# Performance work log

Hardware: AMD Instinct MI355X
Metric: run time of the kernel (lower is better)

Reference implementation:

```python
import jax, jax.numpy as jnp
import numpy as np

B, TP, TH = 128, 128, 64
V, E, H, O = 50000, 300, 512, 3


def _lstm(x, lens, Wih, Whh, bih, bhh):
    # PyTorch LSTM, batch_first, gate order i,f,g,o; masked like pack_padded_sequence
    Bn, T, _ = x.shape
    Hn = Whh.shape[1]
    mask = jnp.arange(T)[None, :] < lens[:, None]  # [B,T]
    def step(carry, xt_mt):
        h, c = carry
        xt, mt = xt_mt  # [B,E], [B,1]
        g = xt @ Wih.T + h @ Whh.T + bih + bhh
        i, f, gg, o = jnp.split(g, 4, axis=-1)
        c_new = jax.nn.sigmoid(f) * c + jax.nn.sigmoid(i) * jnp.tanh(gg)
        h_new = jax.nn.sigmoid(o) * jnp.tanh(c_new)
        return (jnp.where(mt, h_new, h), jnp.where(mt, c_new, c)), jnp.where(mt, h_new, 0.0)
    z = jnp.zeros((Bn, Hn), x.dtype)
    _, hs = jax.lax.scan(step, (z, z), (jnp.swapaxes(x, 0, 1), jnp.swapaxes(mask, 0, 1)[..., None]))
    return jnp.swapaxes(hs, 0, 1)  # [B,T,H]


def _cell(x, h, c, Wih, Whh, bih, bhh):
    g = x @ Wih.T + h @ Whh.T + bih + bhh
    i, f, gg, o = jnp.split(g, 4, axis=-1)
    c_new = jax.nn.sigmoid(f) * c + jax.nn.sigmoid(i) * jnp.tanh(gg)
    h_new = jax.nn.sigmoid(o) * jnp.tanh(c_new)
    return h_new, c_new


def setup_inputs() -> dict:
    key = jax.random.key(0)
    ks = jax.random.split(key, 24)
    def unif(k, shape, fan):
        s = 1.0 / np.sqrt(fan)
        return jax.random.uniform(k, shape, jnp.float32, -s, s)
    inp = {}
    inp["premise"] = jax.random.randint(ks[0], (B, TP), 0, V, jnp.int32)
    inp["premise_len"] = jnp.full((B,), TP, jnp.int32)
    inp["hypothesis"] = jax.random.randint(ks[1], (B, TH), 0, V, jnp.int32)
    inp["hypothesis_len"] = jnp.full((B,), TH, jnp.int32)
    inp["embed_table"] = jax.random.normal(ks[2], (V, E), jnp.float32) * 0.1
    inp["embed_table"] = inp["embed_table"].at[0].set(0.0)  # padding_idx=0
    # premise LSTM
    inp["Wih_p"] = unif(ks[3], (4 * H, E), H); inp["Whh_p"] = unif(ks[4], (4 * H, H), H)
    inp["bih_p"] = unif(ks[5], (4 * H,), H); inp["bhh_p"] = unif(ks[6], (4 * H,), H)
    # hypothesis LSTM
    inp["Wih_h"] = unif(ks[7], (4 * H, E), H); inp["Whh_h"] = unif(ks[8], (4 * H, H), H)
    inp["bih_h"] = unif(ks[9], (4 * H,), H); inp["bhh_h"] = unif(ks[10], (4 * H,), H)
    # match LSTMCell (input 2H)
    inp["Wih_m"] = unif(ks[11], (4 * H, 2 * H), H); inp["Whh_m"] = unif(ks[12], (4 * H, H), H)
    inp["bih_m"] = unif(ks[13], (4 * H,), H); inp["bhh_m"] = unif(ks[14], (4 * H,), H)
    # attention
    inp["w_e"] = jax.random.uniform(ks[15], (H,), jnp.float32, 0.0, 1.0)
    inp["W_s"] = unif(ks[16], (H, H), H)
    inp["W_t"] = unif(ks[17], (H, H), H)
    inp["W_m"] = unif(ks[18], (H, H), H)
    inp["W_fc"] = unif(ks[19], (O, H), H)
    inp["b_fc"] = unif(ks[20], (O,), H)
    return inp


def reference(premise, premise_len, hypothesis, hypothesis_len, embed_table,
              Wih_p, Whh_p, bih_p, bhh_p, Wih_h, Whh_h, bih_h, bhh_h,
              Wih_m, Whh_m, bih_m, bhh_m, w_e, W_s, W_t, W_m, W_fc, b_fc):
    Bn = premise.shape[0]
    Hn = Whh_m.shape[1]
    p_emb = embed_table[premise]      # [B,Tp,E]
    h_emb = embed_table[hypothesis]   # [B,Th,E]
    h_s = _lstm(p_emb, premise_len, Wih_p, Whh_p, bih_p, bhh_p)      # [B,Tp,H]
    h_t = _lstm(h_emb, hypothesis_len, Wih_h, Whh_h, bih_h, bhh_h)   # [B,Th,H]
    Ws = jnp.einsum('bth,gh->btg', h_s, W_s)  # precompute w_s(h_s) once

    def step(carry, htk):
        h_m, c_m = carry
        q = htk @ W_t.T + h_m @ W_m.T                    # [B,H]
        s = jnp.tanh(Ws + q[:, None, :])                 # [B,Tp,H]
        e = s @ w_e                                      # [B,Tp]
        alpha = jax.nn.softmax(e, axis=1)                # softmax over premise positions
        a = jnp.einsum('bt,bth->bh', alpha, h_s)
        m_k = jnp.concatenate([a, htk], axis=1)          # [B,2H]
        h_m2, c_m2 = _cell(m_k, h_m, c_m, Wih_m, Whh_m, bih_m, bhh_m)
        return (h_m2, c_m2), h_m2

    z = jnp.zeros((Bn, Hn), h_s.dtype)
    _, hm_all = jax.lax.scan(step, (z, z), jnp.swapaxes(h_t, 0, 1))  # [Th,B,H]
    hm_all = jnp.swapaxes(hm_all, 0, 1)                              # [B,Th,H]
    idx = (hypothesis_len - 1).astype(jnp.int32)[:, None, None]
    last = jnp.take_along_axis(hm_all, idx, axis=1)[:, 0, :]         # last hidden per example
    return last @ W_fc.T + b_fc
```

## Files before the change

### kernel.cpp

```cpp
#include <hip/hip_runtime.h>

constexpr int BB = 128;
constexpr int TPp = 128;
constexpr int THh = 64;
constexpr int HH = 512;

constexpr size_t OFF_HS     = 0;
constexpr size_t SZ_HS      = (size_t)16384 * 512;
constexpr size_t OFF_HT     = OFF_HS + SZ_HS;
constexpr size_t SZ_HT      = (size_t)8192 * 512;
constexpr size_t OFF_WSM    = OFF_HT + SZ_HT;
constexpr size_t SZ_WSM     = (size_t)16384 * 512;
constexpr size_t OFF_WIHT_P = OFF_WSM + SZ_WSM;
constexpr size_t SZ_WIHT    = (size_t)304 * 2048;
constexpr size_t OFF_WIHT_H = OFF_WIHT_P + SZ_WIHT;
constexpr size_t OFF_WHHT_P = OFF_WIHT_H + SZ_WIHT;
constexpr size_t OFF_WHHT_H = OFF_WHHT_P + (size_t)512 * 2048;
constexpr size_t OFF_WB1T   = OFF_WHHT_H + (size_t)512 * 2048;
constexpr size_t OFF_WIA    = OFF_WB1T + (size_t)2560 * 1024;
constexpr size_t OFF_WEF    = OFF_WIA + (size_t)2048 * 512;
constexpr size_t OFF_BM     = OFF_WEF + 512;
constexpr size_t OFF_HC_P   = OFF_BM + 2048;
constexpr size_t OFF_HC_H   = OFF_HC_P + 2 * (size_t)BB * HH;
constexpr size_t OFF_C_P    = OFF_HC_H + 2 * (size_t)BB * HH;
constexpr size_t OFF_C_H    = OFF_C_P + (size_t)BB * HH;
constexpr size_t OFF_Q      = OFF_C_H + (size_t)BB * HH;
constexpr size_t OFF_GH     = OFF_Q + (size_t)BB * HH;
constexpr size_t OFF_A      = OFF_GH + (size_t)BB * 2048;
constexpr size_t OFF_HM     = OFF_A + (size_t)BB * HH;
constexpr size_t OFF_CM     = OFF_HM + (size_t)BB * HH;
constexpr size_t OFF_LAST   = OFF_CM + (size_t)BB * HH;
constexpr size_t OFF_BARP   = OFF_LAST + (size_t)BB * HH;
constexpr size_t OFF_BARH   = OFF_BARP + 2560;
constexpr size_t OFF_BARF   = OFF_BARH + 2560;
constexpr size_t OFF_BARM   = OFF_BARF + 4352;
constexpr size_t WS_FLOATS  = OFF_BARM + 4352;

__device__ __forceinline__ float sigmf(float x) { return 1.0f / (1.0f + __expf(-x)); }
__device__ __forceinline__ float tanh_f(float x) {
  float e = __expf(-2.0f * fabsf(x));
  float r = (1.0f - e) / (1.0f + e);
  return copysignf(r, x);
}

__device__ __forceinline__ float aload4(const float* p) {
  unsigned u = __hip_atomic_load((const unsigned*)p, __ATOMIC_RELAXED, __HIP_MEMORY_SCOPE_AGENT);
  return __uint_as_float(u);
}
__device__ __forceinline__ void astore4(float* p, float v) {
  __hip_atomic_store((unsigned*)p, __float_as_uint(v), __ATOMIC_RELAXED, __HIP_MEMORY_SCOPE_AGENT);
}
__device__ __forceinline__ float4 aload16(const float* p) {
  const unsigned long long* q = (const unsigned long long*)p;
  unsigned long long u0 = __hip_atomic_load(q, __ATOMIC_RELAXED, __HIP_MEMORY_SCOPE_AGENT);
  unsigned long long u1 = __hip_atomic_load(q + 1, __ATOMIC_RELAXED, __HIP_MEMORY_SCOPE_AGENT);
  union { unsigned long long u; float2 f; } c0, c1;
  c0.u = u0; c1.u = u1;
  float4 f; f.x = c0.f.x; f.y = c0.f.y; f.z = c1.f.x; f.w = c1.f.y;
  return f;
}

__device__ __forceinline__ void gbar3(unsigned* bar, int ep, int base, int n) {
  asm volatile("s_waitcnt vmcnt(0) lgkmcnt(0)" ::: "memory");
  __syncthreads();
  const int tid = threadIdx.x;
  const int rel = (int)blockIdx.x - base;
  if (tid == 0)
    __hip_atomic_store(bar + (size_t)rel * 16, (unsigned)ep,
                       __ATOMIC_RELAXED, __HIP_MEMORY_SCOPE_AGENT);
  if (rel == 0) {
    for (int s = tid; s < n; s += (int)blockDim.x)
      while (__hip_atomic_load(bar + (size_t)s * 16,
                               __ATOMIC_RELAXED, __HIP_MEMORY_SCOPE_AGENT) < (unsigned)ep)
        __builtin_amdgcn_s_sleep(1);
    __syncthreads();
    if (tid == 0)
      __hip_atomic_store(bar + (size_t)n * 16, (unsigned)ep,
                         __ATOMIC_RELAXED, __HIP_MEMORY_SCOPE_AGENT);
  } else if (tid == 0) {
    while (__hip_atomic_load(bar + (size_t)n * 16,
                             __ATOMIC_RELAXED, __HIP_MEMORY_SCOPE_AGENT) < (unsigned)ep)
      __builtin_amdgcn_s_sleep(1);
  }
  __syncthreads();
}

__global__ void k_diag(float* out, float v) {
  int i = blockIdx.x * 64 + threadIdx.x;
  if (i < BB * 3) out[i] = v;
}

__global__ __launch_bounds__(256) void k_prep(float* ws,
    const float* Wih_p, const float* bih_p, const float* bhh_p,
    const float* Wih_h, const float* bih_h, const float* bhh_h,
    const float* Whh_p, const float* Whh_h,
    const float* Whh_m, const float* Wih_m, const float* bih_m, const float* bhh_m,
    const float* W_m, const float* W_t, const float* w_e) {
  size_t gid = (size_t)blockIdx.x * 256 + threadIdx.x;
  if (gid < SZ_WIHT) {
    int k = (int)(gid >> 11), r = (int)(gid & 2047);
    float v = (k < 300) ? Wih_p[(size_t)r * 300 + k]
            : (k == 303) ? (bih_p[r] + bhh_p[r]) : 0.f;
    ws[OFF_WIHT_P + gid] = v;
    return;
  }
  gid -= SZ_WIHT;
  if (gid < SZ_WIHT) {
    int k = (int)(gid >> 11), r = (int)(gid & 2047);
    float v = (k < 300) ? Wih_h[(size_t)r * 300 + k]
            : (k == 303) ? (bih_h[r] + bhh_h[r]) : 0.f;
    ws[OFF_WIHT_H + gid] = v;
    return;
  }
  gid -= SZ_WIHT;
  const size_t NT = (size_t)512 * 2048;
  if (gid < NT) {
    int li = (int)(gid >> 13);
    int rem = (int)(gid & 8191);
    int k = rem >> 4, c = rem & 15;
    int jj = c >> 2, g = c & 3;
    ws[OFF_WHHT_P + gid] = Whh_p[(size_t)(g * 512 + li * 4 + jj) * 512 + k];
    return;
  }
  gid -= NT;
  if (gid < NT) {
    int li = (int)(gid >> 13);
    int rem = (int)(gid & 8191);
    int k = rem >> 4, c = rem & 15;
    int jj = c >> 2, g = c & 3;
    ws[OFF_WHHT_H + gid] = Whh_h[(size_t)(g * 512 + li * 4 + jj) * 512 + k];
    return;
  }
  gid -= NT;
  if (gid < (size_t)2560 * 1024) {
    int c = (int)(gid >> 10), k = (int)(gid & 1023);
    float v;
    if (c < 512) {
      v = (k < 512) ? W_m[(size_t)c * 512 + k] : W_t[(size_t)c * 512 + (k - 512)];
    } else {
      int p = c - 512;
      int j = p >> 2, g = p & 3;
      int r = g * 512 + j;
      v = (k < 512) ? Whh_m[(size_t)r * 512 + k] : Wih_m[(size_t)r * 1024 + k];
    }
    ws[OFF_WB1T + gid] = v;
    return;
  }
  gid -= (size_t)2560 * 1024;
  if (gid < (size_t)2048 * 512) {
    int c = (int)(gid >> 9), k = (int)(gid & 511);
    int j = c >> 2, g = c & 3;
    ws[OFF_WIA + gid] = Wih_m[((size_t)g * 512 + j) * 1024 + k];
    return;
  }
  gid -= (size_t)2048 * 512;
  if (gid < 512) { ws[OFF_WEF + gid] = w_e[gid]; return; }
  gid -= 512;
  if (gid < 2048) { ws[OFF_BM + gid] = bih_m[gid] + bhh_m[gid]; return; }
  gid -= 2048;
  if (gid < (size_t)393216) { ws[OFF_HC_P + gid] = 0.f; return; }
  gid -= 393216;
  if (gid < (size_t)131072) { ws[OFF_HM + gid] = 0.f; return; }
  gid -= 131072;
  if (gid < 13824) { ws[OFF_BARP + gid] = 0.f; return; }
}

__global__ __launch_bounds__(256) void k_gemm(const float* __restrict__ A,
                                              const float* __restrict__ Bw, int ldb, int Kdim,
                                              int N, float* __restrict__ C, int ntilesN) {
  __shared__ float As[16][68];
  __shared__ float Bs[16][68];
  const int tid = threadIdx.x;
  const int bid = blockIdx.x;
  const int tm = bid / ntilesN, tn = bid % ntilesN;
  const int m0 = tm * 64, n0 = tn * 64;
  const int tx = tid & 15, ty = tid >> 4;
  const int srow = tid >> 2, skc = (tid & 3) * 4;
  float acc[4][4] = {};
  const float* arowf = A + (size_t)(m0 + srow) * Kdim;
  const float* brow = Bw + (size_t)(n0 + srow) * ldb;
  for (int k0 = 0; k0 < Kdim; k0 += 16) {
    float4 v = *(const float4*)(arowf + k0 + skc);
    As[skc + 0][srow] = v.x; As[skc + 1][srow] = v.y;
    As[skc + 2][srow] = v.z; As[skc + 3][srow] = v.w;
#pragma unroll
    for (int i = 0; i < 4; i++) Bs[skc + i][srow] = brow[k0 + skc + i];
    __syncthreads();
#pragma unroll
    for (int kk = 0; kk < 16; kk++) {
      float4 a4 = *(float4*)&As[kk][ty * 4];
      float4 b4 = *(float4*)&Bs[kk][tx * 4];
      acc[0][0] += a4.x * b4.x; acc[0][1] += a4.x * b4.y; acc[0][2] += a4.x * b4.z; acc[0][3] += a4.x * b4.w;
      acc[1][0] += a4.y * b4.x; acc[1][1] += a4.y * b4.y; acc[1][2] += a4.y * b4.z; acc[1][3] += a4.y * b4.w;
      acc[2][0] += a4.z * b4.x; acc[2][1] += a4.z * b4.y; acc[2][2] += a4.z * b4.z; acc[2][3] += a4.z * b4.w;
      acc[3][0] += a4.w * b4.x; acc[3][1] += a4.w * b4.y; acc[3][2] += a4.w * b4.z; acc[3][3] += a4.w * b4.w;
    }
    __syncthreads();
  }
  const int m = m0 + ty * 4, n = n0 + tx * 4;
#pragma unroll
  for (int i = 0; i < 4; i++) {
    float4 o = {acc[i][0], acc[i][1], acc[i][2], acc[i][3]};
    *(float4*)&C[(size_t)(m + i) * N + n] = o;
  }
}

__global__ __launch_bounds__(512) void k_lstm_mega(float* __restrict__ ws,
    const int* __restrict__ premise, const int* __restrict__ hyp,
    const int* __restrict__ plen, const int* __restrict__ hlen,
    const float* __restrict__ emb) {
  __shared__ float4 wlds4[2048];
  __shared__ float4 scr4[2048];
  float* Bx = (float*)wlds4;
  float* Alds = (float*)scr4;

  const int tid = threadIdx.x;
  const int bid = blockIdx.x;
  const int seq = bid >> 7;
  const int li = bid & 127;
  const int T = seq ? THh : TPp;
  const int* toks = seq ? hyp : premise;
  const int* lens = seq ? hlen : plen;
  const float* wstk = ws + (seq ? OFF_WHHT_H : OFF_WHHT_P) + (size_t)li * 8192;
  const float* WX = ws + (seq ? OFF_WIHT_H : OFF_WIHT_P);
  float* hc = ws + (seq ? OFF_HC_H : OFF_HC_P);
  float* xg = ws + OFF_WSM + (size_t)bid * 32768;
  unsigned* barS = (unsigned*)(ws + (seq ? OFF_BARH : OFF_BARP));
  const int sbase = seq ? 128 : 0;

  const int w = tid >> 6, lane = tid & 63;
  const int cg = w & 3, bh = w >> 2;
  const int b = bh * 64 + lane;
  const int sw = b & 7;
  const int jcol = li * 4 + cg;
  const int len = lens[b];
  float c_r = 0.f, h_r = 0.f;
  int epS = 1;
  int sb[4], sk[4];
#pragma unroll
  for (int j2 = 0; j2 < 4; j2++) { int fi = tid + j2 * 512; sb[j2] = fi >> 4; sk[j2] = fi & 15; }
  const int kofs = (tid & 3) * 4;

  for (int t = 0; t < T; t++) {
    if ((t & 15) == 0) {
      __syncthreads();
      for (int i = tid; i < 16 * 304; i += 512) {
        int c = i / 304, kk = i - c * 304;
        int jj = c >> 2, g = c & 3;
        Bx[i] = WX[(size_t)kk * 2048 + g * 512 + li * 4 + jj];
      }
      __syncthreads();
      for (int rg = 0; rg < 4; rg++) {
        int tk[4];
#pragma unroll
        for (int j2 = 0; j2 < 4; j2++) {
          int rl = (tid >> 2) + j2 * 128;
          int R = rg * 512 + rl;
          int tl = R >> 7, bb = R & 127;
          tk[j2] = toks[(size_t)bb * T + t + tl];
        }
        float4 pa[4];
#pragma unroll
        for (int j2 = 0; j2 < 4; j2++) {
          if (kofs + 3 < 300) pa[j2] = *(const float4*)(emb + (size_t)tk[j2] * 300 + kofs);
          else { float4 z = {0.f, 0.f, 0.f, 0.f}; pa[j2] = z; }
        }
        float acc[16];
#pragma unroll
        for (int c = 0; c < 16; c++) acc[c] = 0.f;
        for (int ck = 0; ck < 19; ck++) {
          __syncthreads();
#pragma unroll
          for (int j2 = 0; j2 < 4; j2++) {
            int fi = tid + j2 * 512;
            *(float4*)&Alds[(fi >> 2) * 16 + kofs] = pa[j2];
          }
          __syncthreads();
          if (ck < 18) {
            int kb = (ck + 1) * 16 + kofs;
#pragma unroll
            for (int j2 = 0; j2 < 4; j2++) {
              if (kb + 3 < 300) {
                pa[j2] = *(const float4*)(emb + (size_t)tk[j2] * 300 + kb);
              } else {
                float v0 = (kb + 0 < 300) ? emb[(size_t)tk[j2] * 300 + kb + 0] : (kb + 0 == 303 ? 1.f : 0.f);
                float v1 = (kb + 1 < 300) ? emb[(size_t)tk[j2] * 300 + kb + 1] : (kb + 1 == 303 ? 1.f : 0.f);
                float v2 = (kb + 2 < 300) ? emb[(size_t)tk[j2] * 300 + kb + 2] : (kb + 2 == 303 ? 1.f : 0.f);
                float v3 = (kb + 3 < 300) ? emb[(size_t)tk[j2] * 300 + kb + 3] : (kb + 3 == 303 ? 1.f : 0.f);
                float4 z = {v0, v1, v2, v3}; pa[j2] = z;
              }
            }
          }
          int kb0 = ck * 16;
#pragma unroll
          for (int kk4 = 0; kk4 < 4; kk4++) {
            float4 av = *(float4*)&Alds[tid * 16 + kk4 * 4];
#pragma unroll
            for (int c = 0; c < 16; c++) {
              float4 bv = *(float4*)&Bx[c * 304 + kb0 + kk4 * 4];
              acc[c] += av.x * bv.x + av.y * bv.y + av.z * bv.z + av.w * bv.w;
            }
          }
        }
        int R = rg * 512 + tid;
#pragma unroll
        for (int cq = 0; cq < 4; cq++) {
          float4 o = {acc[cq * 4], acc[cq * 4 + 1], acc[cq * 4 + 2], acc[cq * 4 + 3]};
          *(float4*)&xg[(size_t)R * 16 + cq * 4] = o;
        }
      }
      __syncthreads();
      {
        const float4* src = (const float4*)wstk;
#pragma unroll
        for (int j2 = 0; j2 < 4; j2++) wlds4[tid + j2 * 512] = src[tid + j2 * 512];
      }
    }
    {
      const int par = t & 1;
      const float* hin = hc + (size_t)par * (BB * HH);
      float* hout = hc + (size_t)(par ^ 1) * (BB * HH);
      float4 acc = {0.f, 0.f, 0.f, 0.f};
      float4 pre[4];
#pragma unroll
      for (int j2 = 0; j2 < 4; j2++)
        pre[j2] = aload16(hin + (size_t)sb[j2] * 512 + sk[j2] * 4);
      for (int kc = 0; kc < 512; kc += 64) {
        __syncthreads();
#pragma unroll
        for (int j2 = 0; j2 < 4; j2++)
          scr4[sb[j2] * 16 + (sk[j2] ^ (sb[j2] & 7))] = pre[j2];
        __syncthreads();
        if (kc + 64 < 512) {
#pragma unroll
          for (int j2 = 0; j2 < 4; j2++)
            pre[j2] = aload16(hin + (size_t)sb[j2] * 512 + (kc + 64) + sk[j2] * 4);
        }
#pragma unroll
        for (int kk = 0; kk < 64; kk += 4) {
          int k4 = kk >> 2;
          float4 h4 = scr4[b * 16 + (k4 ^ sw)];
          float4 w0 = wlds4[(kc + kk + 0) * 4 + cg];
          float4 w1 = wlds4[(kc + kk + 1) * 4 + cg];
          float4 w2 = wlds4[(kc + kk + 2) * 4 + cg];
          float4 w3 = wlds4[(kc + kk + 3) * 4 + cg];
          acc.x += h4.x * w0.x + h4.y * w1.x + h4.z * w2.x + h4.w * w3.x;
          acc.y += h4.x * w0.y + h4.y * w1.y + h4.z * w2.y + h4.w * w3.y;
          acc.z += h4.x * w0.z + h4.y * w1.z + h4.z * w2.z + h4.w * w3.z;
          acc.w += h4.x * w0.w + h4.y * w1.w + h4.z * w2.w + h4.w * w3.w;
        }
      }
      float4 x0 = *(const float4*)&xg[(((size_t)(t & 15)) * 128 + b) * 16 + cg * 4];
      float iv = sigmf(acc.x + x0.x), fv = sigmf(acc.y + x0.y);
      float gv = tanh_f(acc.z + x0.z), ov = sigmf(acc.w + x0.w);
      float cn = fv * c_r + iv * gv;
      float hn = ov * tanh_f(cn);
      bool inr = t < len;
      if (inr) { c_r = cn; h_r = hn; }
      if (!seq) ws[OFF_HS + ((size_t)b * TPp + t) * 512 + jcol] = inr ? hn : 0.f;
      else      ws[OFF_HT + ((size_t)b * THh + t) * 512 + jcol] = inr ? hn : 0.f;
      astore4(hout + (size_t)b * 512 + jcol, h_r);
      gbar3(barS, epS, sbase, 128); epS++;
    }
  }
}

__global__ __launch_bounds__(512) void k_match_mega(float* __restrict__ ws,
                                                    const int* __restrict__ hlen) {
  __shared__ float smem[16384];
  float* B1 = smem;
  float* W3 = smem + 10240;
  float4* AL4 = (float4*)(smem + 14336);
  float* SCR = smem + 14336;

  const int tid = threadIdx.x;
  const int bid = blockIdx.x;
  float* hm = ws + OFF_HM;
  const float* ht = ws + OFF_HT;
  float* qT = ws + OFF_Q;
  float* ghT = ws + OFF_GH;
  float* abuf = ws + OFF_A;
  float* last = ws + OFF_LAST;
  unsigned* barM = (unsigned*)(ws + OFF_BARM);

  {
    const float* src = ws + OFF_WB1T + (size_t)bid * 10240;
    for (int i = tid; i < 10240; i += 512) B1[i] = src[i];
    const float* s2 = ws + OFF_WIA + (size_t)bid * 4096;
    for (int i = tid; i < 4096; i += 512) W3[i] = s2[i];
  }
  const int r = tid & 127;
  const int khh = (tid >> 7) & 1;
  const int h5 = tid >> 8;
  const int j3 = bid * 2 + h5;
  const int skh = tid >> 8, sq4 = (tid >> 7) & 1, sbv = tid & 127;
  float c_reg = 0.f;
  float bmp[4];
#pragma unroll
  for (int g = 0; g < 4; g++) bmp[g] = ws[OFF_BM + g * 512 + j3];
  const int hl = hlen[r];
  int ep = 1;
  __syncthreads();

  for (int k = 0; k < THh; k++) {
    {
      float acc[5] = {0.f, 0.f, 0.f, 0.f, 0.f};
      float4 p = (skh == 0) ? aload16(&hm[(size_t)sbv * 512 + sq4 * 4])
                            : *(const float4*)&ht[((size_t)sbv * THh + k) * 512 + sq4 * 4];
      for (int ch = 0; ch < 64; ch++) {
        __syncthreads();
        AL4[skh * 256 + sq4 * 128 + sbv] = p;
        __syncthreads();
        if (ch < 63) {
          int kn = (ch + 1) * 8 + sq4 * 4;
          p = (skh == 0) ? aload16(&hm[(size_t)sbv * 512 + kn])
                         : *(const float4*)&ht[((size_t)sbv * THh + k) * 512 + kn];
        }
        const int kb = khh * 512 + ch * 8;
#pragma unroll
        for (int q4 = 0; q4 < 2; q4++) {
          float4 av = AL4[khh * 256 + q4 * 128 + r];
#pragma unroll
          for (int cc = 0; cc < 5; cc++) {
            float4 bv = *(float4*)&B1[(h5 * 5 + cc) * 1024 + kb + q4 * 4];
            acc[cc] += av.x * bv.x + av.y * bv.y + av.z * bv.z + av.w * bv.w;
          }
        }
      }
      __syncthreads();
      if (khh == 1) {
#pragma unroll
        for (int cc = 0; cc < 5; cc++) SCR[(h5 * 5 + cc) * 128 + r] = acc[cc];
      }
      __syncthreads();
      if (khh == 0) {
#pragma unroll
        for (int cc = 0; cc < 5; cc++) {
          float val = acc[cc] + SCR[(h5 * 5 + cc) * 128 + r];
          int c = bid * 10 + h5 * 5 + cc;
          if (c < 512) astore4(&qT[(size_t)c * 128 + r], val);
          else astore4(&ghT[(size_t)(c - 512) * 128 + r], val);
        }
      }
    }
    gbar3(barM, ep, 0, 256); ep++;
    if (bid < 128) {
      float* q_lds = SCR; float* we_lds = SCR + 512; float* e_part = SCR + 1024;
      float* e_lds = SCR + 1536; float* alpha_lds = SCR + 1664; float* red_s = SCR + 1792;
      const int b = bid;
      const float* Wsb = ws + OFF_WSM;
      const float* hs = ws + OFF_HS;
      q_lds[tid] = aload4(&qT[(size_t)tid * 128 + b]);
      we_lds[tid] = ws[OFF_WEF + tid];
      __syncthreads();
      {
        int t2 = tid >> 2;
        int gbase = (tid & 3) * 128;
        const float* wsrow = Wsb + ((size_t)b * TPp + t2) * 512 + gbase;
        float s = 0.f;
        for (int ii = 0; ii < 128; ii += 4) {
          float4 wv = *(const float4*)(wsrow + ii);
          float4 qv = *(float4*)&q_lds[gbase + ii];
          float4 ev = *(float4*)&we_lds[gbase + ii];
          s += tanh_f(wv.x + qv.x) * ev.x + tanh_f(wv.y + qv.y) * ev.y +
               tanh_f(wv.z + qv.z) * ev.z + tanh_f(wv.w + qv.w) * ev.w;
        }
        e_part[tid] = s;
      }
      __syncthreads();
      if (tid < 128)
        e_lds[tid] = e_part[tid * 4] + e_part[tid * 4 + 1] + e_part[tid * 4 + 2] + e_part[tid * 4 + 3];
      __syncthreads();
      if (tid < 64) {
        float m = fmaxf(e_lds[tid], e_lds[tid + 64]);
        for (int off = 32; off > 0; off >>= 1) m = fmaxf(m, __shfl_down(m, off));
        if (tid == 0) red_s[0] = m;
      }
      __syncthreads();
      if (tid < 128) alpha_lds[tid] = __expf(e_lds[tid] - red_s[0]);
      __syncthreads();
      if (tid < 64) {
        float s = alpha_lds[tid] + alpha_lds[tid + 64];
        for (int off = 32; off > 0; off >>= 1) s += __shfl_down(s, off);
        if (tid == 0) red_s[1] = 1.f / s;
      }
      __syncthreads();
      {
        float inv = red_s[1];
        float a0 = 0.f;
        const float* hsb = hs + (size_t)b * TPp * 512 + tid;
        for (int t2 = 0; t2 < TPp; t2++) a0 += alpha_lds[t2] * hsb[(size_t)t2 * 512];
        astore4(&abuf[(size_t)b * 512 + tid], a0 * inv);
      }
    }
    gbar3(barM, ep, 0, 256); ep++;
    {
      float acc3[4] = {0.f, 0.f, 0.f, 0.f};
      float4 p3 = aload16(&abuf[(size_t)sbv * 512 + skh * 256 + sq4 * 4]);
      for (int ch = 0; ch < 32; ch++) {
        __syncthreads();
        AL4[skh * 256 + sq4 * 128 + sbv] = p3;
        __syncthreads();
        if (ch < 31) {
          int kn = skh * 256 + (ch + 1) * 8 + sq4 * 4;
          p3 = aload16(&abuf[(size_t)sbv * 512 + kn]);
        }
        const int kb = khh * 256 + ch * 8;
#pragma unroll
        for (int q4 = 0; q4 < 2; q4++) {
          float4 av = AL4[khh * 256 + q4 * 128 + r];
#pragma unroll
          for (int cc = 0; cc < 4; cc++) {
            float4 wv = *(float4*)&W3[(h5 * 4 + cc) * 512 + kb + q4 * 4];
            acc3[cc] += av.x * wv.x + av.y * wv.y + av.z * wv.z + av.w * wv.w;
          }
        }
      }
      __syncthreads();
      if (khh == 1) {
#pragma unroll
        for (int cc = 0; cc < 4; cc++) SCR[(h5 * 4 + cc) * 128 + r] = acc3[cc];
      }
      __syncthreads();
      if (khh == 0) {
        float g4[4];
#pragma unroll
        for (int g = 0; g < 4; g++) {
          g4[g] = acc3[g] + SCR[(h5 * 4 + g) * 128 + r] +
                  aload4(&ghT[(size_t)(j3 * 4 + g) * 128 + r]) + bmp[g];
        }
        float iv = sigmf(g4[0]), fv = sigmf(g4[1]), gg = tanh_f(g4[2]), ov = sigmf(g4[3]);
        float cn = fv * c_reg + iv * gg;
        float hn = ov * tanh_f(cn);
        c_reg = cn;
        astore4(&hm[(size_t)r * 512 + j3], hn);
        if (k == hl - 1) last[(size_t)r * 512 + j3] = hn;
      }
    }
    gbar3(barM, ep, 0, 256); ep++;
  }
}

__global__ __launch_bounds__(256) void k_fc(const float* __restrict__ ws, const float* __restrict__ Wfc,
                                            const float* __restrict__ bfc, float* __restrict__ out) {
  int idx = blockIdx.x * 256 + threadIdx.x;
  if (idx >= BB * 3) return;
  int b = idx / 3, o = idx - b * 3;
  const float* lrow = ws + OFF_LAST + (size_t)b * 512;
  const float* wrow = Wfc + (size_t)o * 512;
  float acc = bfc[o];
  for (int h = 0; h < 512; h++) acc += lrow[h] * wrow[h];
  out[idx] = acc;
}

extern "C" void kernel_launch(void* const* d_in, const int* in_sizes, int n_in, void* d_out,
                              int out_size, void* d_ws, size_t ws_size, hipStream_t stream) {
  const int* premise = (const int*)d_in[0];
  const int* plen = (const int*)d_in[1];
  const int* hyp = (const int*)d_in[2];
  const int* hlen = (const int*)d_in[3];
  const float* emb = (const float*)d_in[4];
  const float* Wih_p = (const float*)d_in[5];
  const float* Whh_p = (const float*)d_in[6];
  const float* bih_p = (const float*)d_in[7];
  const float* bhh_p = (const float*)d_in[8];
  const float* Wih_h = (const float*)d_in[9];
  const float* Whh_h = (const float*)d_in[10];
  const float* bih_h = (const float*)d_in[11];
  const float* bhh_h = (const float*)d_in[12];
  const float* Wih_m = (const float*)d_in[13];
  const float* Whh_m = (const float*)d_in[14];
  const float* bih_m = (const float*)d_in[15];
  const float* bhh_m = (const float*)d_in[16];
  const float* w_e = (const float*)d_in[17];
  const float* W_s = (const float*)d_in[18];
  const float* W_t = (const float*)d_in[19];
  const float* W_m = (const float*)d_in[20];
  const float* W_fc = (const float*)d_in[21];
  const float* b_fc = (const float*)d_in[22];
  float* ws = (float*)d_ws;
  float* out = (float*)d_out;

  if (ws_size < WS_FLOATS * sizeof(float)) {
    float mb = (float)((double)ws_size / (1024.0 * 1024.0));
    k_diag<<<dim3(6), dim3(64), 0, stream>>>(out, mb);
    return;
  }

  {
    size_t total = 2 * SZ_WIHT + 2 * (size_t)512 * 2048 + (size_t)2560 * 1024 +
                   (size_t)2048 * 512 + 512 + 2048 + 393216 + 131072 + 13824;
    int nb = (int)((total + 255) / 256);
    k_prep<<<dim3(nb), dim3(256), 0, stream>>>(ws, Wih_p, bih_p, bhh_p, Wih_h, bih_h, bhh_h,
                                               Whh_p, Whh_h, Whh_m, Wih_m, bih_m, bhh_m,
                                               W_m, W_t, w_e);
  }
  {
    void* args[] = {(void*)&ws, (void*)&premise, (void*)&hyp, (void*)&plen, (void*)&hlen, (void*)&emb};
    hipError_t e = hipLaunchCooperativeKernel((const void*)k_lstm_mega, dim3(256), dim3(512),
                                              args, 0, stream);
    if (e != hipSuccess)
      k_lstm_mega<<<dim3(256), dim3(512), 0, stream>>>(ws, premise, hyp, plen, hlen, emb);
  }
  k_gemm<<<dim3(256 * 8), dim3(256), 0, stream>>>(ws + OFF_HS, W_s, 512, 512, 512,
                                                  ws + OFF_WSM, 8);
  {
    void* args[] = {(void*)&ws, (void*)&hlen};
    hipError_t e = hipLaunchCooperativeKernel((const void*)k_match_mega, dim3(256), dim3(512),
                                              args, 0, stream);
    if (e != hipSuccess)
      k_match_mega<<<dim3(256), dim3(512), 0, stream>>>(ws, hlen);
  }
  k_fc<<<dim3(2), dim3(256), 0, stream>>>(ws, W_fc, b_fc, out);
}
```

Baseline: 11.81 ms.

## Partition recurrent kernels by batch groups with local barriers instead of global

Both persistent kernels (LSTM and match) are re-partitioned so each block group owns a slice of batch rows (16 rows) and a slice of gate columns. Grid barriers then only span the 16 or 32 blocks of a group instead of all 128 or 256 blocks, since batch rows are independent. Recurrent weights are now streamed from global/L2 each step instead of kept resident in LDS. The input projection is computed cooperatively as a tiled GEMM across the group. The goal is lower barrier latency per timestep, paid for with more global weight traffic per step.

Measured after the change: 13.06 ms. 10.6% more time.

```diff
diff --git a/kernel.cpp b/kernel.cpp
--- a/kernel.cpp
+++ b/kernel.cpp
@@ -59,18 +59,25 @@
   float4 f; f.x = c0.f.x; f.y = c0.f.y; f.z = c1.f.x; f.w = c1.f.y;
   return f;
 }
-
-__device__ __forceinline__ void gbar3(unsigned* bar, int ep, int base, int n) {
+__device__ __forceinline__ void astore16(float* p, float4 v) {
+  union { unsigned long long u; float2 f; } c0, c1;
+  c0.f.x = v.x; c0.f.y = v.y; c1.f.x = v.z; c1.f.y = v.w;
+  unsigned long long* q = (unsigned long long*)p;
+  __hip_atomic_store(q, c0.u, __ATOMIC_RELAXED, __HIP_MEMORY_SCOPE_AGENT);
+  __hip_atomic_store(q + 1, c1.u, __ATOMIC_RELAXED, __HIP_MEMORY_SCOPE_AGENT);
+}
+
+__device__ __forceinline__ void gbarD(unsigned* bar, int ep, int first, int n) {
   asm volatile("s_waitcnt vmcnt(0) lgkmcnt(0)" ::: "memory");
   __syncthreads();
   const int tid = threadIdx.x;
-  const int rel = (int)blockIdx.x - base;
+  const int rel = (int)blockIdx.x - first;
   if (tid == 0)
     __hip_atomic_store(bar + (size_t)rel * 16, (unsigned)ep,
                        __ATOMIC_RELAXED, __HIP_MEMORY_SCOPE_AGENT);
   if (rel == 0) {
-    for (int s = tid; s < n; s += (int)blockDim.x)
-      while (__hip_atomic_load(bar + (size_t)s * 16,
+    if (tid < n)
+      while (__hip_atomic_load(bar + (size_t)tid * 16,
                                __ATOMIC_RELAXED, __HIP_MEMORY_SCOPE_AGENT) < (unsigned)ep)
         __builtin_amdgcn_s_sleep(1);
     __syncthreads();
@@ -83,6 +90,12 @@
       __builtin_amdgcn_s_sleep(1);
   }
   __syncthreads();
+}
+
+__device__ __forceinline__ float red4(float v) {
+  v += __shfl_down(v, 16, 64);
+  v += __shfl_down(v, 32, 64);
+  return v;
 }
 
 __global__ void k_diag(float* out, float v) {
@@ -115,20 +128,16 @@
   gid -= SZ_WIHT;
   const size_t NT = (size_t)512 * 2048;
   if (gid < NT) {
-    int li = (int)(gid >> 13);
-    int rem = (int)(gid & 8191);
-    int k = rem >> 4, c = rem & 15;
-    int jj = c >> 2, g = c & 3;
-    ws[OFF_WHHT_P + gid] = Whh_p[(size_t)(g * 512 + li * 4 + jj) * 512 + k];
+    int c = (int)(gid >> 9), kk = (int)(gid & 511);
+    int j = c >> 2, g = c & 3;
+    ws[OFF_WHHT_P + gid] = Whh_p[(size_t)(g * 512 + j) * 512 + kk];
     return;
   }
   gid -= NT;
   if (gid < NT) {
-    int li = (int)(gid >> 13);
-    int rem = (int)(gid & 8191);
-    int k = rem >> 4, c = rem & 15;
-    int jj = c >> 2, g = c & 3;
-    ws[OFF_WHHT_H + gid] = Whh_h[(size_t)(g * 512 + li * 4 + jj) * 512 + k];
+    int c = (int)(gid >> 9), kk = (int)(gid & 511);
+    int j = c >> 2, g = c & 3;
+    ws[OFF_WHHT_H + gid] = Whh_h[(size_t)(g * 512 + j) * 512 + kk];
     return;
   }
   gid -= NT;
@@ -209,248 +218,223 @@
     const int* __restrict__ premise, const int* __restrict__ hyp,
     const int* __restrict__ plen, const int* __restrict__ hlen,
     const float* __restrict__ emb) {
-  __shared__ float4 wlds4[2048];
-  __shared__ float4 scr4[2048];
-  float* Bx = (float*)wlds4;
-  float* Alds = (float*)scr4;
+  __shared__ float4 smem4[4096];
+  float4* Alds4 = smem4;
+  float* xAs = (float*)(smem4 + 2048);
+  float* xBs = xAs + 16 * 68;
+  int* xTok = (int*)(xBs + 16 * 68);
 
   const int tid = threadIdx.x;
   const int bid = blockIdx.x;
   const int seq = bid >> 7;
-  const int li = bid & 127;
+  const int u = bid & 127;
+  const int gb = u >> 4, gj = u & 15;
   const int T = seq ? THh : TPp;
   const int* toks = seq ? hyp : premise;
   const int* lens = seq ? hlen : plen;
-  const float* wstk = ws + (seq ? OFF_WHHT_H : OFF_WHHT_P) + (size_t)li * 8192;
+  const float* WL = ws + (seq ? OFF_WHHT_H : OFF_WHHT_P);
   const float* WX = ws + (seq ? OFF_WIHT_H : OFF_WIHT_P);
   float* hc = ws + (seq ? OFF_HC_H : OFF_HC_P);
-  float* xg = ws + OFF_WSM + (size_t)bid * 32768;
-  unsigned* barS = (unsigned*)(ws + (seq ? OFF_BARH : OFF_BARP));
-  const int sbase = seq ? 128 : 0;
+  float* hsout = ws + (seq ? OFF_HT : OFF_HS);
+  float* xgd = ws + OFF_WSM + (size_t)(seq * 8 + gb) * (16 * 16 * 2048);
+  unsigned* bar = (unsigned*)(ws + (seq ? OFF_BARH : OFF_BARP)) + gb * 272;
+  const int dfirst = seq * 128 + gb * 16;
 
   const int w = tid >> 6, lane = tid & 63;
-  const int cg = w & 3, bh = w >> 2;
-  const int b = bh * 64 + lane;
-  const int sw = b & 7;
-  const int jcol = li * 4 + cg;
-  const int len = lens[b];
-  float c_r = 0.f, h_r = 0.f;
-  int epS = 1;
-  int sb[4], sk[4];
-#pragma unroll
-  for (int j2 = 0; j2 < 4; j2++) { int fi = tid + j2 * 512; sb[j2] = fi >> 4; sk[j2] = fi & 15; }
-  const int kofs = (tid & 3) * 4;
+  const int b_loc = lane & 15, kq = lane >> 4;
+  const int b_glob = gb * 16 + b_loc;
+  const int c0 = gj * 128 + w * 16;
+  const int j0 = c0 >> 2;
+  const int len = lens[b_glob];
+  float c_r[4] = {0.f, 0.f, 0.f, 0.f}, h_r[4] = {0.f, 0.f, 0.f, 0.f};
+  int ep = 1;
 
   for (int t = 0; t < T; t++) {
     if ((t & 15) == 0) {
-      __syncthreads();
-      for (int i = tid; i < 16 * 304; i += 512) {
-        int c = i / 304, kk = i - c * 304;
-        int jj = c >> 2, g = c & 3;
-        Bx[i] = WX[(size_t)kk * 2048 + g * 512 + li * 4 + jj];
-      }
-      __syncthreads();
-      for (int rg = 0; rg < 4; rg++) {
-        int tk[4];
-#pragma unroll
-        for (int j2 = 0; j2 < 4; j2++) {
-          int rl = (tid >> 2) + j2 * 128;
-          int R = rg * 512 + rl;
-          int tl = R >> 7, bb = R & 127;
-          tk[j2] = toks[(size_t)bb * T + t + tl];
-        }
-        float4 pa[4];
-#pragma unroll
-        for (int j2 = 0; j2 < 4; j2++) {
-          if (kofs + 3 < 300) pa[j2] = *(const float4*)(emb + (size_t)tk[j2] * 300 + kofs);
-          else { float4 z = {0.f, 0.f, 0.f, 0.f}; pa[j2] = z; }
-        }
-        float acc[16];
-#pragma unroll
-        for (int c = 0; c < 16; c++) acc[c] = 0.f;
-        for (int ck = 0; ck < 19; ck++) {
-          __syncthreads();
-#pragma unroll
-          for (int j2 = 0; j2 < 4; j2++) {
-            int fi = tid + j2 * 512;
-            *(float4*)&Alds[(fi >> 2) * 16 + kofs] = pa[j2];
+      for (int ti = gj; ti < 128; ti += 16) {
+        const int tm = ti >> 5, tn = ti & 31;
+        const int m0 = tm * 64, n0 = tn * 64;
+        if (tid < 64) {
+          int rr = m0 + tid;
+          int tl = rr >> 4, bl = rr & 15;
+          xTok[tid] = toks[(size_t)(gb * 16 + bl) * T + t + tl];
+        }
+        __syncthreads();
+        const int sr = tid & 63, sk2 = (tid >> 6) * 2;
+        const int tx = tid & 15, ty = tid >> 4;
+        float acc2[2][4] = {};
+        for (int k0 = 0; k0 < 304; k0 += 16) {
+          int tok = xTok[sr];
+#pragma unroll
+          for (int i = 0; i < 2; i++) {
+            int kx = k0 + sk2 + i;
+            float v = 0.f;
+            if (kx < 300) v = emb[(size_t)tok * 300 + kx];
+            else if (kx == 303) v = 1.0f;
+            xAs[(sk2 + i) * 68 + sr] = v;
+          }
+#pragma unroll
+          for (int s = 0; s < 2; s++) {
+            int i2 = tid + s * 512;
+            int kb = i2 >> 6, nb = i2 & 63;
+            xBs[kb * 68 + nb] = WX[(size_t)(k0 + kb) * 2048 + n0 + nb];
           }
           __syncthreads();
-          if (ck < 18) {
-            int kb = (ck + 1) * 16 + kofs;
-#pragma unroll
-            for (int j2 = 0; j2 < 4; j2++) {
-              if (kb + 3 < 300) {
-                pa[j2] = *(const float4*)(emb + (size_t)tk[j2] * 300 + kb);
-              } else {
-                float v0 = (kb + 0 < 300) ? emb[(size_t)tk[j2] * 300 + kb + 0] : (kb + 0 == 303 ? 1.f : 0.f);
-                float v1 = (kb + 1 < 300) ? emb[(size_t)tk[j2] * 300 + kb + 1] : (kb + 1 == 303 ? 1.f : 0.f);
-                float v2 = (kb + 2 < 300) ? emb[(size_t)tk[j2] * 300 + kb + 2] : (kb + 2 == 303 ? 1.f : 0.f);
-                float v3 = (kb + 3 < 300) ? emb[(size_t)tk[j2] * 300 + kb + 3] : (kb + 3 == 303 ? 1.f : 0.f);
-                float4 z = {v0, v1, v2, v3}; pa[j2] = z;
-              }
-            }
+#pragma unroll
+          for (int kk = 0; kk < 16; kk++) {
+            float a0 = xAs[kk * 68 + ty * 2];
+            float a1 = xAs[kk * 68 + ty * 2 + 1];
+            float4 b4 = *(float4*)&xBs[kk * 68 + tx * 4];
+            acc2[0][0] += a0 * b4.x; acc2[0][1] += a0 * b4.y; acc2[0][2] += a0 * b4.z; acc2[0][3] += a0 * b4.w;
+            acc2[1][0] += a1 * b4.x; acc2[1][1] += a1 * b4.y; acc2[1][2] += a1 * b4.z; acc2[1][3] += a1 * b4.w;
           }
-          int kb0 = ck * 16;
-#pragma unroll
-          for (int kk4 = 0; kk4 < 4; kk4++) {
-            float4 av = *(float4*)&Alds[tid * 16 + kk4 * 4];
-#pragma unroll
-            for (int c = 0; c < 16; c++) {
-              float4 bv = *(float4*)&Bx[c * 304 + kb0 + kk4 * 4];
-              acc[c] += av.x * bv.x + av.y * bv.y + av.z * bv.z + av.w * bv.w;
-            }
+          __syncthreads();
+        }
+#pragma unroll
+        for (int i = 0; i < 2; i++) {
+          int rr = m0 + ty * 2 + i;
+          int tl = rr >> 4, bl = rr & 15;
+          float* dst = xgd + ((size_t)tl * 16 + bl) * 2048;
+#pragma unroll
+          for (int jj = 0; jj < 4; jj++) {
+            int cI = n0 + tx * 4 + jj;
+            int g = cI >> 9, j = cI & 511;
+            astore4(dst + j * 4 + g, acc2[i][jj]);
           }
         }
-        int R = rg * 512 + tid;
-#pragma unroll
-        for (int cq = 0; cq < 4; cq++) {
-          float4 o = {acc[cq * 4], acc[cq * 4 + 1], acc[cq * 4 + 2], acc[cq * 4 + 3]};
-          *(float4*)&xg[(size_t)R * 16 + cq * 4] = o;
-        }
-      }
-      __syncthreads();
-      {
-        const float4* src = (const float4*)wstk;
-#pragma unroll
-        for (int j2 = 0; j2 < 4; j2++) wlds4[tid + j2 * 512] = src[tid + j2 * 512];
-      }
+      }
+      gbarD(bar, ep, dfirst, 16); ep++;
     }
     {
-      const int par = t & 1;
-      const float* hin = hc + (size_t)par * (BB * HH);
-      float* hout = hc + (size_t)(par ^ 1) * (BB * HH);
-      float4 acc = {0.f, 0.f, 0.f, 0.f};
-      float4 pre[4];
-#pragma unroll
-      for (int j2 = 0; j2 < 4; j2++)
-        pre[j2] = aload16(hin + (size_t)sb[j2] * 512 + sk[j2] * 4);
-      for (int kc = 0; kc < 512; kc += 64) {
-        __syncthreads();
-#pragma unroll
-        for (int j2 = 0; j2 < 4; j2++)
-          scr4[sb[j2] * 16 + (sk[j2] ^ (sb[j2] & 7))] = pre[j2];
-        __syncthreads();
-        if (kc + 64 < 512) {
-#pragma unroll
-          for (int j2 = 0; j2 < 4; j2++)
-            pre[j2] = aload16(hin + (size_t)sb[j2] * 512 + (kc + 64) + sk[j2] * 4);
-        }
-#pragma unroll
-        for (int kk = 0; kk < 64; kk += 4) {
-          int k4 = kk >> 2;
-          float4 h4 = scr4[b * 16 + (k4 ^ sw)];
-          float4 w0 = wlds4[(kc + kk + 0) * 4 + cg];
-          float4 w1 = wlds4[(kc + kk + 1) * 4 + cg];
-          float4 w2 = wlds4[(kc + kk + 2) * 4 + cg];
-          float4 w3 = wlds4[(kc + kk + 3) * 4 + cg];
-          acc.x += h4.x * w0.x + h4.y * w1.x + h4.z * w2.x + h4.w * w3.x;
-          acc.y += h4.x * w0.y + h4.y * w1.y + h4.z * w2.y + h4.w * w3.y;
-          acc.z += h4.x * w0.z + h4.y * w1.z + h4.z * w2.z + h4.w * w3.z;
-          acc.w += h4.x * w0.w + h4.y * w1.w + h4.z * w2.w + h4.w * w3.w;
-        }
-      }
-      float4 x0 = *(const float4*)&xg[(((size_t)(t & 15)) * 128 + b) * 16 + cg * 4];
-      float iv = sigmf(acc.x + x0.x), fv = sigmf(acc.y + x0.y);
-      float gv = tanh_f(acc.z + x0.z), ov = sigmf(acc.w + x0.w);
-      float cn = fv * c_r + iv * gv;
-      float hn = ov * tanh_f(cn);
-      bool inr = t < len;
-      if (inr) { c_r = cn; h_r = hn; }
-      if (!seq) ws[OFF_HS + ((size_t)b * TPp + t) * 512 + jcol] = inr ? hn : 0.f;
-      else      ws[OFF_HT + ((size_t)b * THh + t) * 512 + jcol] = inr ? hn : 0.f;
-      astore4(hout + (size_t)b * 512 + jcol, h_r);
-      gbar3(barS, epS, sbase, 128); epS++;
+      const float* hin = hc + (size_t)(t & 1) * (BB * HH);
+      float* hout = hc + (size_t)((t + 1) & 1) * (BB * HH);
+#pragma unroll
+      for (int i = 0; i < 4; i++) {
+        int f = tid + 512 * i;
+        int bl = f >> 7, k4 = f & 127;
+        Alds4[bl * 128 + (k4 ^ (bl & 7))] = aload16(hin + (size_t)(gb * 16 + bl) * 512 + k4 * 4);
+      }
+      __syncthreads();
+      float acc[16];
+#pragma unroll
+      for (int c = 0; c < 16; c++) acc[c] = 0.f;
+      for (int it = 0; it < 32; it++) {
+        int kk = it * 16 + kq * 4;
+        float4 a4 = Alds4[b_loc * 128 + ((it * 4 + kq) ^ (b_loc & 7))];
+#pragma unroll
+        for (int cq = 0; cq < 16; cq++) {
+          float4 w4 = *(const float4*)&WL[(size_t)(c0 + cq) * 512 + kk];
+          acc[cq] += a4.x * w4.x + a4.y * w4.y + a4.z * w4.z + a4.w * w4.w;
+        }
+      }
+#pragma unroll
+      for (int cq = 0; cq < 16; cq++) acc[cq] = red4(acc[cq]);
+      if (kq == 0) {
+        const float* xb = xgd + ((size_t)(t & 15) * 16 + b_loc) * 2048 + c0;
+        float4 hv;
+        float* hvp = (float*)&hv;
+        bool inr = t < len;
+#pragma unroll
+        for (int jl = 0; jl < 4; jl++) {
+          float4 xa = aload16(xb + jl * 4);
+          float iv = sigmf(acc[jl * 4 + 0] + xa.x);
+          float fv = sigmf(acc[jl * 4 + 1] + xa.y);
+          float gv = tanh_f(acc[jl * 4 + 2] + xa.z);
+          float ov = sigmf(acc[jl * 4 + 3] + xa.w);
+          float cn = fv * c_r[jl] + iv * gv;
+          float hn = ov * tanh_f(cn);
+          if (inr) { c_r[jl] = cn; h_r[jl] = hn; }
+          hvp[jl] = inr ? hn : 0.f;
+        }
+        *(float4*)(hsout + ((size_t)b_glob * T + t) * 512 + j0) = hv;
+        float4 ho = {h_r[0], h_r[1], h_r[2], h_r[3]};
+        astore16(hout + (size_t)b_glob * 512 + j0, ho);
+      }
+      gbarD(bar, ep, dfirst, 16); ep++;
     }
   }
 }
 
 __global__ __launch_bounds__(512) void k_match_mega(float* __restrict__ ws,
                                                     const int* __restrict__ hlen) {
-  __shared__ float smem[16384];
-  float* B1 = smem;
-  float* W3 = smem + 10240;
-  float4* AL4 = (float4*)(smem + 14336);
-  float* SCR = smem + 14336;
+  __shared__ float4 smem4[4096];
+  float4* A1 = smem4;
+  float4* A3 = smem4;
+  float* SC = (float*)smem4;
 
   const int tid = threadIdx.x;
   const int bid = blockIdx.x;
+  const int gr = bid >> 5, gc = bid & 31;
+  const int dfirst = gr * 32;
+  unsigned* bar = (unsigned*)(ws + OFF_BARM) + gr * 528;
+
   float* hm = ws + OFF_HM;
   const float* ht = ws + OFF_HT;
-  float* qT = ws + OFF_Q;
-  float* ghT = ws + OFF_GH;
+  float* q = ws + OFF_Q;
+  float* gh = ws + OFF_GH;
   float* abuf = ws + OFF_A;
   float* last = ws + OFF_LAST;
-  unsigned* barM = (unsigned*)(ws + OFF_BARM);
-
-  {
-    const float* src = ws + OFF_WB1T + (size_t)bid * 10240;
-    for (int i = tid; i < 10240; i += 512) B1[i] = src[i];
-    const float* s2 = ws + OFF_WIA + (size_t)bid * 4096;
-    for (int i = tid; i < 4096; i += 512) W3[i] = s2[i];
-  }
-  const int r = tid & 127;
-  const int khh = (tid >> 7) & 1;
-  const int h5 = tid >> 8;
-  const int j3 = bid * 2 + h5;
-  const int skh = tid >> 8, sq4 = (tid >> 7) & 1, sbv = tid & 127;
-  float c_reg = 0.f;
-  float bmp[4];
-#pragma unroll
-  for (int g = 0; g < 4; g++) bmp[g] = ws[OFF_BM + g * 512 + j3];
-  const int hl = hlen[r];
+  const float* B1 = ws + OFF_WB1T;
+  const float* W3 = ws + OFF_WIA;
+
+  const int w = tid >> 6, lane = tid & 63;
+  const int rl = lane & 15, kq = lane >> 4;
+  const int r_g = gr * 16 + rl;
+  const int c0p = gc * 80 + w * 10;
+  const int c0q = gc * 64 + w * 8;
+  const int jq = c0q >> 2;
+  float c_reg[2] = {0.f, 0.f};
+  const int hl = hlen[r_g];
+  float bmp[8];
+#pragma unroll
+  for (int jl = 0; jl < 2; jl++)
+#pragma unroll
+    for (int g = 0; g < 4; g++) bmp[jl * 4 + g] = ws[OFF_BM + g * 512 + jq + jl];
   int ep = 1;
-  __syncthreads();
 
   for (int k = 0; k < THh; k++) {
     {
-      float acc[5] = {0.f, 0.f, 0.f, 0.f, 0.f};
-      float4 p = (skh == 0) ? aload16(&hm[(size_t)sbv * 512 + sq4 * 4])
-                            : *(const float4*)&ht[((size_t)sbv * THh + k) * 512 + sq4 * 4];
-      for (int ch = 0; ch < 64; ch++) {
-        __syncthreads();
-        AL4[skh * 256 + sq4 * 128 + sbv] = p;
-        __syncthreads();
-        if (ch < 63) {
-          int kn = (ch + 1) * 8 + sq4 * 4;
-          p = (skh == 0) ? aload16(&hm[(size_t)sbv * 512 + kn])
-                         : *(const float4*)&ht[((size_t)sbv * THh + k) * 512 + kn];
-        }
-        const int kb = khh * 512 + ch * 8;
-#pragma unroll
-        for (int q4 = 0; q4 < 2; q4++) {
-          float4 av = AL4[khh * 256 + q4 * 128 + r];
-#pragma unroll
-          for (int cc = 0; cc < 5; cc++) {
-            float4 bv = *(float4*)&B1[(h5 * 5 + cc) * 1024 + kb + q4 * 4];
-            acc[cc] += av.x * bv.x + av.y * bv.y + av.z * bv.z + av.w * bv.w;
-          }
-        }
-      }
-      __syncthreads();
-      if (khh == 1) {
-#pragma unroll
-        for (int cc = 0; cc < 5; cc++) SCR[(h5 * 5 + cc) * 128 + r] = acc[cc];
-      }
-      __syncthreads();
-      if (khh == 0) {
-#pragma unroll
-        for (int cc = 0; cc < 5; cc++) {
-          float val = acc[cc] + SCR[(h5 * 5 + cc) * 128 + r];
-          int c = bid * 10 + h5 * 5 + cc;
-          if (c < 512) astore4(&qT[(size_t)c * 128 + r], val);
-          else astore4(&ghT[(size_t)(c - 512) * 128 + r], val);
-        }
-      }
-    }
-    gbar3(barM, ep, 0, 256); ep++;
-    if (bid < 128) {
-      float* q_lds = SCR; float* we_lds = SCR + 512; float* e_part = SCR + 1024;
-      float* e_lds = SCR + 1536; float* alpha_lds = SCR + 1664; float* red_s = SCR + 1792;
-      const int b = bid;
+#pragma unroll
+      for (int i = 0; i < 8; i++) {
+        int f = tid + 512 * i;
+        int rr = f >> 8, k4 = f & 255;
+        float4 v;
+        if (k4 < 128) v = aload16(&hm[(size_t)(gr * 16 + rr) * 512 + k4 * 4]);
+        else v = *(const float4*)&ht[((size_t)(gr * 16 + rr) * THh + k) * 512 + (k4 - 128) * 4];
+        A1[rr * 256 + (k4 ^ (rr & 7))] = v;
+      }
+      __syncthreads();
+      float acc[10];
+#pragma unroll
+      for (int cc = 0; cc < 10; cc++) acc[cc] = 0.f;
+      for (int it = 0; it < 64; it++) {
+        int kk = it * 16 + kq * 4;
+        float4 a4 = A1[rl * 256 + ((it * 4 + kq) ^ (rl & 7))];
+#pragma unroll
+        for (int cc = 0; cc < 10; cc++) {
+          float4 b4 = *(const float4*)&B1[(size_t)(c0p + cc) * 1024 + kk];
+          acc[cc] += a4.x * b4.x + a4.y * b4.y + a4.z * b4.z + a4.w * b4.w;
+        }
+      }
+#pragma unroll
+      for (int cc = 0; cc < 10; cc++) acc[cc] = red4(acc[cc]);
+      if (kq == 0) {
+#pragma unroll
+        for (int cc = 0; cc < 10; cc++) {
+          int c = c0p + cc;
+          if (c < 512) astore4(&q[(size_t)r_g * 512 + c], acc[cc]);
+          else astore4(&gh[(size_t)r_g * 2048 + (c - 512)], acc[cc]);
+        }
+      }
+    }
+    gbarD(bar, ep, dfirst, 32); ep++;
+    if (gc < 16) {
+      const int b = gr * 16 + gc;
+      float* q_lds = SC; float* we_lds = SC + 512; float* e_part = SC + 1024;
+      float* e_lds = SC + 1536; float* alpha_lds = SC + 1664; float* red_s = SC + 1792;
       const float* Wsb = ws + OFF_WSM;
       const float* hs = ws + OFF_HS;
-      q_lds[tid] = aload4(&qT[(size_t)tid * 128 + b]);
+      q_lds[tid] = aload4(&q[(size_t)b * 512 + tid]);
       we_lds[tid] = ws[OFF_WEF + tid];
       __syncthreads();
       {
@@ -493,51 +477,46 @@
         astore4(&abuf[(size_t)b * 512 + tid], a0 * inv);
       }
     }
-    gbar3(barM, ep, 0, 256); ep++;
+    gbarD(bar, ep, dfirst, 32); ep++;
     {
-      float acc3[4] = {0.f, 0.f, 0.f, 0.f};
-      float4 p3 = aload16(&abuf[(size_t)sbv * 512 + skh * 256 + sq4 * 4]);
-      for (int ch = 0; ch < 32; ch++) {
-        __syncthreads();
-        AL4[skh * 256 + sq4 * 128 + sbv] = p3;
-        __syncthreads();
-        if (ch < 31) {
-          int kn = skh * 256 + (ch + 1) * 8 + sq4 * 4;
-          p3 = aload16(&abuf[(size_t)sbv * 512 + kn]);
-        }
-        const int kb = khh * 256 + ch * 8;
-#pragma unroll
-        for (int q4 = 0; q4 < 2; q4++) {
-          float4 av = AL4[khh * 256 + q4 * 128 + r];
-#pragma unroll
-          for (int cc = 0; cc < 4; cc++) {
-            float4 wv = *(float4*)&W3[(h5 * 4 + cc) * 512 + kb + q4 * 4];
-            acc3[cc] += av.x * wv.x + av.y * wv.y + av.z * wv.z + av.w * wv.w;
-          }
-        }
-      }
-      __syncthreads();
-      if (khh == 1) {
-#pragma unroll
-        for (int cc = 0; cc < 4; cc++) SCR[(h5 * 4 + cc) * 128 + r] = acc3[cc];
-      }
-      __syncthreads();
-      if (khh == 0) {
-        float g4[4];
-#pragma unroll
-        for (int g = 0; g < 4; g++) {
-          g4[g] = acc3[g] + SCR[(h5 * 4 + g) * 128 + r] +
-                  aload4(&ghT[(size_t)(j3 * 4 + g) * 128 + r]) + bmp[g];
-        }
-        float iv = sigmf(g4[0]), fv = sigmf(g4[1]), gg = tanh_f(g4[2]), ov = sigmf(g4[3]);
-        float cn = fv * c_reg + iv * gg;
-        float hn = ov * tanh_f(cn);
-        c_reg = cn;
-        astore4(&hm[(size_t)r * 512 + j3], hn);
-        if (k == hl - 1) last[(size_t)r * 512 + j3] = hn;
-      }
-    }
-    gbar3(barM, ep, 0, 256); ep++;
+#pragma unroll
+      for (int i = 0; i < 4; i++) {
+        int f = tid + 512 * i;
+        int rr = f >> 7, k4 = f & 127;
+        A3[rr * 128 + (k4 ^ (rr & 7))] = aload16(&abuf[(size_t)(gr * 16 + rr) * 512 + k4 * 4]);
+      }
+      __syncthreads();
+      float acc[8];
+#pragma unroll
+      for (int cc = 0; cc < 8; cc++) acc[cc] = 0.f;
+      for (int it = 0; it < 32; it++) {
+        int kk = it * 16 + kq * 4;
+        float4 a4 = A3[rl * 128 + ((it * 4 + kq) ^ (rl & 7))];
+#pragma unroll
+        for (int cc = 0; cc < 8; cc++) {
+          float4 w4 = *(const float4*)&W3[(size_t)(c0q + cc) * 512 + kk];
+          acc[cc] += a4.x * w4.x + a4.y * w4.y + a4.z * w4.z + a4.w * w4.w;
+        }
+      }
+#pragma unroll
+      for (int cc = 0; cc < 8; cc++) acc[cc] = red4(acc[cc]);
+      if (kq == 0) {
+#pragma unroll
+        for (int jl = 0; jl < 2; jl++) {
+          float4 gh4 = aload16(&gh[(size_t)r_g * 2048 + c0q + jl * 4]);
+          float iv = sigmf(acc[jl * 4 + 0] + gh4.x + bmp[jl * 4 + 0]);
+          float fv = sigmf(acc[jl * 4 + 1] + gh4.y + bmp[jl * 4 + 1]);
+          float gv = tanh_f(acc[jl * 4 + 2] + gh4.z + bmp[jl * 4 + 2]);
+          float ov = sigmf(acc[jl * 4 + 3] + gh4.w + bmp[jl * 4 + 3]);
+          float cn = fv * c_reg[jl] + iv * gv;
+          float hn = ov * tanh_f(cn);
+          c_reg[jl] = cn;
+          astore4(&hm[(size_t)r_g * 512 + jq + jl], hn);
+          if (k == hl - 1) last[(size_t)r_g * 512 + jq + jl] = hn;
+        }
+      }
+    }
+    gbarD(bar, ep, dfirst, 32); ep++;
   }
 }
 
```
